# Performance work log

Hardware: AMD Instinct MI355X
Metric: run time of the kernel (lower is better)

Reference implementation:

```python
import jax, jax.numpy as jnp
import numpy as np

EPS = 1e-5

def _conv1d(x, w, b):
    # x: [N, Cin, L], w: [Cout, Cin, 3], SAME padding (pad=1)
    y = jax.lax.conv_general_dilated(
        x, w, window_strides=(1,), padding=((1, 1),),
        dimension_numbers=("NCH", "OIH", "NCH"))
    return y + b[None, :, None]

def _bn(x, gamma, beta, mean, var):
    # inference-mode BatchNorm1d over channel dim
    inv = gamma / jnp.sqrt(var + EPS)
    return x * inv[None, :, None] + (beta - mean * inv)[None, :, None]

def _make_params(key):
    ks = jax.random.split(key, 9)
    def w(k, o, i):
        return jax.random.normal(k, (o, i, 3), jnp.float32) * (1.0 / np.sqrt(i * 3))
    p = {}
    p["w1"], p["b1"] = w(ks[0], 128, 1), jnp.zeros((128,), jnp.float32)
    p["w2"], p["b2"] = w(ks[1], 256, 128), jnp.zeros((256,), jnp.float32)
    p["w3"], p["b3"] = w(ks[2], 256, 256), jnp.zeros((256,), jnp.float32)
    for i, c in zip((1, 2, 3), (128, 256, 256)):
        p[f"g{i}"] = jnp.ones((c,), jnp.float32)
        p[f"be{i}"] = jnp.zeros((c,), jnp.float32)
        p[f"m{i}"] = jax.random.normal(ks[2 + i], (c,), jnp.float32) * 0.1
        p[f"v{i}"] = 1.0 + 0.1 * jax.random.uniform(ks[5 + i], (c,), jnp.float32)
    return p

def setup_inputs() -> dict:
    key = jax.random.key(0)
    kx, kp = jax.random.split(key)
    inp = {"x": jax.random.normal(kx, (16, 64, 520), jnp.float32)}
    inp.update(_make_params(kp))
    return inp

def reference(x, w1, b1, w2, b2, w3, b3,
              g1, be1, m1, v1, g2, be2, m2, v2, g3, be3, m3, v3):
    B, T, D = x.shape
    h = x.reshape(B * T, 1, D)                     # fuse time into batch
    h = jax.nn.relu(_bn(_conv1d(h, w1, b1), g1, be1, m1, v1))
    h = jax.nn.relu(_bn(_conv1d(h, w2, b2), g2, be2, m2, v2))
    h = jax.nn.relu(_bn(_conv1d(h, w3, b3), g3, be3, m3, v3))
    out = h.mean(axis=-1)                          # AdaptiveAvgPool1d(1) + squeeze
    return out.reshape(B, T, -1)                   # [B, T, feature_dim]
```

## Files before the change

### kernel.cpp

```cpp
#include <hip/hip_runtime.h>
#include <hip/hip_bf16.h>

#define EPSV 1e-5f

typedef __attribute__((ext_vector_type(8))) short short8;
typedef __attribute__((ext_vector_type(4))) short short4v;
typedef __attribute__((ext_vector_type(4))) float f32x4;

static __device__ __forceinline__ short f2bf(float f) {
    unsigned int u = __builtin_bit_cast(unsigned int, f);
    unsigned int r = (u + 0x7FFFu + ((u >> 16) & 1u)) >> 16;
    return (short)(r & 0xFFFFu);
}
static __device__ __forceinline__ f32x4 zero4() { f32x4 z = {0.f, 0.f, 0.f, 0.f}; return z; }

static __device__ __forceinline__ void gload16(const void* g, void* l) {
    __builtin_amdgcn_global_load_lds((const unsigned int*)g, (unsigned int*)l, 16, 0, 0);
}

__global__ void sfe_prep(
    const float* __restrict__ w1, const float* __restrict__ b1,
    const float* __restrict__ w2, const float* __restrict__ b2,
    const float* __restrict__ w3, const float* __restrict__ b3,
    const float* __restrict__ g1, const float* __restrict__ be1,
    const float* __restrict__ m1, const float* __restrict__ v1,
    const float* __restrict__ g2, const float* __restrict__ be2,
    const float* __restrict__ m2, const float* __restrict__ v2,
    const float* __restrict__ g3, const float* __restrict__ be3,
    const float* __restrict__ m3, const float* __restrict__ v3,
    short* __restrict__ W2f, short* __restrict__ W3f,
    float* __restrict__ s1o, float* __restrict__ bb1o,
    float* __restrict__ bb2o, float* __restrict__ bb3o)
{
    int idx = blockIdx.x * 256 + threadIdx.x;
    int e = idx & 7, lane = (idx >> 3) & 63, ct = (idx >> 9) & 15;
    int lr = lane & 15, lg = lane >> 4;
    {
        int kc = idx >> 13;
        int c3 = ct * 16 + lr;
        int c2in = (kc & 7) * 32 + lg * 8 + e;
        int dk = kc >> 3;
        float s = g3[c3] / sqrtf(v3[c3] + EPSV);
        W3f[idx] = f2bf(w3[(c3 * 256 + c2in) * 3 + dk] * s);
    }
    if (idx < 98304) {
        int kc = idx >> 13;
        int c2 = ct * 16 + lr;
        int ci = (kc & 3) * 32 + lg * 8 + e;
        int dk = kc >> 2;
        float s = g2[c2] / sqrtf(v2[c2] + EPSV);
        W2f[idx] = f2bf(w2[(c2 * 128 + ci) * 3 + dk] * s);
    }
    if (idx < 128) {
        float s = g1[idx] / sqrtf(v1[idx] + EPSV);
        s1o[idx]  = s;
        bb1o[idx] = (b1[idx] - m1[idx]) * s + be1[idx];
    }
    if (idx < 256) {
        float s2 = g2[idx] / sqrtf(v2[idx] + EPSV);
        bb2o[idx] = (b2[idx] - m2[idx]) * s2 + be2[idx];
        float s3 = g3[idx] / sqrtf(v3[idx] + EPSV);
        bb3o[idx] = (b3[idx] - m3[idx]) * s3 + be3[idx];
    }
}

#define MFMA16(A, B, C) __builtin_amdgcn_mfma_f32_16x16x32_bf16(A, B, C, 0, 0, 0)

__global__ __launch_bounds__(512, 1) void sfe_l12(
    const float* __restrict__ x, const float* __restrict__ w1,
    const short* __restrict__ W2f,
    const float* __restrict__ s1a, const float* __restrict__ bb1a,
    const float* __restrict__ bb2a,
    char* __restrict__ h2g, int seq0)
{
    __shared__ __align__(16) char ring[32768];
    __shared__ __align__(16) char obuf[2][16384];
    __shared__ float xs[528];

    const int tid = threadIdx.x, lane = tid & 63, wid = tid >> 6;
    const int lr = lane & 15, lg = lane >> 4;
    const int seq = seq0 + blockIdx.x;
    char* h2b = h2g + (size_t)blockIdx.x * 270336;

    const int c4 = (tid & 31) * 4;
    float w1r[12];
    #pragma unroll
    for (int e2 = 0; e2 < 4; ++e2) {
        w1r[e2 * 3 + 0] = w1[(c4 + e2) * 3 + 0];
        w1r[e2 * 3 + 1] = w1[(c4 + e2) * 3 + 1];
        w1r[e2 * 3 + 2] = w1[(c4 + e2) * 3 + 2];
    }
    const f32x4 s1v = *reinterpret_cast<const f32x4*>(s1a + c4);
    const f32x4 b1v = *reinterpret_cast<const f32x4*>(bb1a + c4);

    short8 W2r[24];
    #pragma unroll
    for (int kc = 0; kc < 12; ++kc) {
        #pragma unroll
        for (int p = 0; p < 2; ++p)
            W2r[kc * 2 + p] = *reinterpret_cast<const short8*>(
                W2f + ((kc * 16 + wid * 2 + p) * 64 + lane) * 8);
    }
    const f32x4 bias0 = *reinterpret_cast<const f32x4*>(bb2a + (wid * 2 + 0) * 16 + lg * 4);
    const f32x4 bias1 = *reinterpret_cast<const f32x4*>(bb2a + (wid * 2 + 1) * 16 + lg * 4);

    for (int i = tid; i < 528; i += 512) {
        int l = i - 1;
        xs[i] = (l >= 0 && l < 520) ? x[(size_t)seq * 520 + l] : 0.f;
    }
    *reinterpret_cast<long long*>(ring + 28672 + tid * 8) = 0ll;
    __syncthreads();

    auto h1chunk = [&](int X) {
        int row = X * 16 + (tid >> 5);
        int rr = (row + 128) & 127;
        short4v hv;
        if (row < 520) {
            float x0 = xs[row], x1 = xs[row + 1], x2 = xs[row + 2];
            #pragma unroll
            for (int e2 = 0; e2 < 4; ++e2) {
                float a = w1r[e2 * 3] * x0 + w1r[e2 * 3 + 1] * x1 + w1r[e2 * 3 + 2] * x2;
                hv[e2] = f2bf(fmaxf(a * s1v[e2] + b1v[e2], 0.f));
            }
        } else {
            hv[0] = 0; hv[1] = 0; hv[2] = 0; hv[3] = 0;
        }
        int ch = c4 >> 3;
        *reinterpret_cast<short4v*>(
            ring + rr * 256 + ((ch ^ (row & 15)) << 4) + (c4 & 7) * 2) = hv;
    };

    h1chunk(0); h1chunk(1); h1chunk(2);
    __syncthreads();

    auto epi = [&](const f32x4& A, int p, const f32x4& bv, int jt, int b) {
        int c2b = (wid * 2 + p) * 16 + lg * 4;
        int ch = c2b >> 3;
        short4v hv;
        #pragma unroll
        for (int r = 0; r < 4; ++r) hv[r] = f2bf(fmaxf(A[r] + bv[r], 0.f));
        *reinterpret_cast<short4v*>(
            obuf[b] + (jt * 16 + lr) * 512 + ((ch ^ lr) << 4) + (c2b & 7) * 2) = hv;
    };

    for (int C = 0; C <= 32; C += 2) {
        const bool do2 = (C < 32);
        const int b = (C >> 1) & 1;
        f32x4 a00 = zero4(), a10 = zero4(), a01 = zero4(), a11 = zero4();
        const int row0base = C * 16 + lr - 1;

        if (do2) {
            #pragma unroll
            for (int kc = 0; kc < 12; ++kc) {
                int dk = kc >> 2, cc = kc & 3;
                int ch = cc * 4 + lg;
                int row0 = row0base + dk, row1 = row0 + 16;
                short8 B0 = *reinterpret_cast<const short8*>(
                    ring + ((row0 + 128) & 127) * 256 + ((ch ^ (row0 & 15)) << 4));
                short8 B1 = *reinterpret_cast<const short8*>(
                    ring + ((row1 + 128) & 127) * 256 + ((ch ^ (row1 & 15)) << 4));
                a00 = MFMA16(W2r[kc * 2 + 0], B0, a00);
                a10 = MFMA16(W2r[kc * 2 + 1], B0, a10);
                a01 = MFMA16(W2r[kc * 2 + 0], B1, a01);
                a11 = MFMA16(W2r[kc * 2 + 1], B1, a11);
            }
        } else {
            #pragma unroll
            for (int kc = 0; kc < 12; ++kc) {
                int dk = kc >> 2, cc = kc & 3;
                int ch = cc * 4 + lg;
                int row0 = row0base + dk;
                short8 B0 = *reinterpret_cast<const short8*>(
                    ring + ((row0 + 128) & 127) * 256 + ((ch ^ (row0 & 15)) << 4));
                a00 = MFMA16(W2r[kc * 2 + 0], B0, a00);
                a10 = MFMA16(W2r[kc * 2 + 1], B0, a10);
            }
        }

        if (C + 3 <= 32) h1chunk(C + 3);
        if (C + 4 <= 32) h1chunk(C + 4);

        epi(a00, 0, bias0, 0, b);
        epi(a10, 1, bias1, 0, b);
        if (do2) { epi(a01, 0, bias0, 1, b); epi(a11, 1, bias1, 1, b); }

        asm volatile("s_waitcnt lgkmcnt(0)" ::: "memory");
        __builtin_amdgcn_s_barrier();

        #pragma unroll
        for (int q = 0; q < 2; ++q) {
            int byteo = q * 8192 + tid * 16;
            int lrow = byteo >> 9;
            int grow = C * 16 + lrow;
            if (grow < 528 && (do2 || lrow < 16)) {
                short8 d = *reinterpret_cast<const short8*>(obuf[b] + byteo);
                if (grow >= 520) { short8 z = {0,0,0,0,0,0,0,0}; d = z; }
                *reinterpret_cast<short8*>(h2b + (size_t)grow * 512 + (byteo & 511)) = d;
            }
        }
    }
}

__global__ __launch_bounds__(256, 1) void sfe_l3(
    const char* __restrict__ h2g, const short* __restrict__ W3f,
    const float* __restrict__ bb3a, float* __restrict__ out, int seq0)
{
    __shared__ __align__(16) char ring[98304];

    const int tid = threadIdx.x, lane = tid & 63, wid = tid >> 6;
    const int lr = lane & 15, lg = lane >> 4;
    const int bi = blockIdx.x;
    const int seq = seq0 + (bi >> 1);
    const int ch2 = bi & 1;
    const char* h2b = h2g + (size_t)(bi >> 1) * 270336;

    short8 W3r[48];
    #pragma unroll
    for (int kc = 0; kc < 24; ++kc) {
        #pragma unroll
        for (int p = 0; p < 2; ++p)
            W3r[kc * 2 + p] = *reinterpret_cast<const short8*>(
                W3f + ((kc * 16 + ch2 * 8 + wid * 2 + p) * 64 + lane) * 8);
    }
    const f32x4 bias0 = *reinterpret_cast<const f32x4*>(bb3a + (ch2 * 8 + wid * 2 + 0) * 16 + lg * 4);
    const f32x4 bias1 = *reinterpret_cast<const f32x4*>(bb3a + (ch2 * 8 + wid * 2 + 1) * 16 + lg * 4);
    f32x4 pool0 = zero4(), pool1 = zero4();

    int Koff[24];
    #pragma unroll
    for (int kc = 0; kc < 24; ++kc) {
        int dk = kc >> 3, cc = kc & 7;
        Koff[kc] = (((cc * 4 + lg) ^ ((lr - 1 + dk) & 15)) << 4);
    }

    auto stage = [&](int X) {
        int Xc = X > 32 ? 32 : X;
        int slot = X % 12;
        #pragma unroll
        for (int q = 0; q < 2; ++q)
            gload16(h2b + Xc * 8192 + q * 4096 + tid * 16,
                    ring + slot * 8192 + q * 4096 + tid * 16);
    };

    #pragma unroll
    for (int q = 0; q < 2; ++q)
        *reinterpret_cast<f32x4*>(ring + 90112 + q * 4096 + tid * 16) = zero4();
    stage(0); stage(1); stage(2); stage(3); stage(4); stage(5); stage(6);
    asm volatile("s_waitcnt vmcnt(4) lgkmcnt(0)" ::: "memory");
    __builtin_amdgcn_s_barrier();

    #define RD(rbarr, KC, JT) \
        (*reinterpret_cast<const short8*>(ring + rbarr[(JT) * 3 + ((KC) >> 3)] + Koff[(KC)]))

    for (int S = 0; S <= 28; S += 4) {
        stage(S + 7); stage(S + 8); stage(S + 9); stage(S + 10);
        __builtin_amdgcn_sched_barrier(0);

        int rb[12];
        #pragma unroll
        for (int jt = 0; jt < 4; ++jt) {
            #pragma unroll
            for (int dk = 0; dk < 3; ++dk)
                rb[jt * 3 + dk] = (((S + jt) * 16 + lr - 1 + dk + 192) % 192) * 512;
        }

        f32x4 a0[4] = {zero4(), zero4(), zero4(), zero4()};
        f32x4 a1[4] = {zero4(), zero4(), zero4(), zero4()};
        short8 Ba[16], Bb[16];

        #define ISSUE(BUF, KCB) \
            _Pragma("unroll") for (int k = 0; k < 4; ++k) { \
                _Pragma("unroll") for (int jt = 0; jt < 4; ++jt) \
                    BUF[k * 4 + jt] = RD(rb, (KCB) + k, jt); \
            } \
            __builtin_amdgcn_sched_barrier(0);

        #define CONSUME(BUF, KCB) \
            _Pragma("unroll") for (int k = 0; k < 4; ++k) { \
                _Pragma("unroll") for (int jt = 0; jt < 4; ++jt) { \
                    a0[jt] = MFMA16(W3r[((KCB) + k) * 2 + 0], BUF[k * 4 + jt], a0[jt]); \
                    a1[jt] = MFMA16(W3r[((KCB) + k) * 2 + 1], BUF[k * 4 + jt], a1[jt]); \
                } \
            } \
            __builtin_amdgcn_sched_barrier(0);

        ISSUE(Ba, 0)
        ISSUE(Bb, 4)
        CONSUME(Ba, 0)
        ISSUE(Ba, 8)
        CONSUME(Bb, 4)
        ISSUE(Bb, 12)
        CONSUME(Ba, 8)
        ISSUE(Ba, 16)
        CONSUME(Bb, 12)
        ISSUE(Bb, 20)
        CONSUME(Ba, 16)
        CONSUME(Bb, 20)

        #undef ISSUE
        #undef CONSUME

        #pragma unroll
        for (int jt = 0; jt < 4; ++jt) {
            f32x4 t0, t1;
            #pragma unroll
            for (int r = 0; r < 4; ++r) {
                t0[r] = fmaxf(a0[jt][r] + bias0[r], 0.f);
                t1[r] = fmaxf(a1[jt][r] + bias1[r], 0.f);
            }
            pool0 += t0;
            pool1 += t1;
        }

        asm volatile("s_waitcnt vmcnt(4) lgkmcnt(0)" ::: "memory");
        __builtin_amdgcn_s_barrier();
    }

    {
        int rbT[3];
        #pragma unroll
        for (int dk = 0; dk < 3; ++dk)
            rbT[dk] = ((512 + lr - 1 + dk + 192) % 192) * 512;

        f32x4 a00 = zero4(), a10 = zero4();
        short8 Ta[12], Tb[12];
        #pragma unroll
        for (int k = 0; k < 12; ++k)
            Ta[k] = *reinterpret_cast<const short8*>(ring + rbT[k >> 3] + Koff[k]);
        __builtin_amdgcn_sched_barrier(0);
        #pragma unroll
        for (int k = 0; k < 12; ++k)
            Tb[k] = *reinterpret_cast<const short8*>(ring + rbT[(k + 12) >> 3] + Koff[k + 12]);
        __builtin_amdgcn_sched_barrier(0);
        #pragma unroll
        for (int k = 0; k < 12; ++k) {
            a00 = MFMA16(W3r[k * 2 + 0], Ta[k], a00);
            a10 = MFMA16(W3r[k * 2 + 1], Ta[k], a10);
        }
        #pragma unroll
        for (int k = 0; k < 12; ++k) {
            a00 = MFMA16(W3r[(k + 12) * 2 + 0], Tb[k], a00);
            a10 = MFMA16(W3r[(k + 12) * 2 + 1], Tb[k], a10);
        }

        bool v0 = (512 + lr) < 520;
        f32x4 t0, t1;
        #pragma unroll
        for (int r = 0; r < 4; ++r) {
            t0[r] = fmaxf(a00[r] + bias0[r], 0.f);
            t1[r] = fmaxf(a10[r] + bias1[r], 0.f);
        }
        pool0 += v0 ? t0 : zero4();
        pool1 += v0 ? t1 : zero4();
    }

    asm volatile("s_waitcnt vmcnt(0)" ::: "memory");

    #pragma unroll
    for (int d = 1; d < 16; d <<= 1) {
        #pragma unroll
        for (int r = 0; r < 4; ++r) {
            pool0[r] += __shfl_xor(pool0[r], d, 64);
            pool1[r] += __shfl_xor(pool1[r], d, 64);
        }
    }
    if (lr == 0) {
        f32x4 o0, o1;
        #pragma unroll
        for (int r = 0; r < 4; ++r) { o0[r] = pool0[r] * (1.f / 520.f); o1[r] = pool1[r] * (1.f / 520.f); }
        *reinterpret_cast<f32x4*>(out + (size_t)seq * 256 + (ch2 * 8 + wid * 2 + 0) * 16 + lg * 4) = o0;
        *reinterpret_cast<f32x4*>(out + (size_t)seq * 256 + (ch2 * 8 + wid * 2 + 1) * 16 + lg * 4) = o1;
    }
}

extern "C" void kernel_launch(void* const* d_in, const int* in_sizes, int n_in,
                              void* d_out, int out_size, void* d_ws, size_t ws_size,
                              hipStream_t stream) {
    (void)n_in; (void)out_size;
    const float* x   = (const float*)d_in[0];
    const float* w1  = (const float*)d_in[1];
    const float* b1  = (const float*)d_in[2];
    const float* w2  = (const float*)d_in[3];
    const float* b2  = (const float*)d_in[4];
    const float* w3  = (const float*)d_in[5];
    const float* b3  = (const float*)d_in[6];
    const float* g1  = (const float*)d_in[7];
    const float* be1 = (const float*)d_in[8];
    const float* m1  = (const float*)d_in[9];
    const float* v1  = (const float*)d_in[10];
    const float* g2  = (const float*)d_in[11];
    const float* be2 = (const float*)d_in[12];
    const float* m2  = (const float*)d_in[13];
    const float* v2  = (const float*)d_in[14];
    const float* g3  = (const float*)d_in[15];
    const float* be3 = (const float*)d_in[16];
    const float* m3  = (const float*)d_in[17];
    const float* v3  = (const float*)d_in[18];

    char* ws = (char*)d_ws;
    short* W2f  = (short*)(ws);
    short* W3f  = (short*)(ws + 196608);
    float* s1o  = (float*)(ws + 589824);
    float* bb1o = (float*)(ws + 590336);
    float* bb2o = (float*)(ws + 590848);
    float* bb3o = (float*)(ws + 591872);
    char*  h2g  = ws + (1 << 20);

    int nseq = in_sizes[0] / 520;
    size_t h2cap = ws_size > (size_t)(1 << 20) ? ws_size - (1 << 20) : 0;
    int maxseq = (int)(h2cap / 270336);
    if (maxseq < 1) maxseq = 1;
    if (maxseq > nseq) maxseq = nseq;

    sfe_prep<<<768, 256, 0, stream>>>(w1, b1, w2, b2, w3, b3,
                                      g1, be1, m1, v1, g2, be2, m2, v2,
                                      g3, be3, m3, v3,
                                      W2f, W3f, s1o, bb1o, bb2o, bb3o);
    for (int s0 = 0; s0 < nseq; s0 += maxseq) {
        int n = (nseq - s0) < maxseq ? (nseq - s0) : maxseq;
        sfe_l12<<<n, 512, 0, stream>>>(x, w1, W2f, s1o, bb1o, bb2o, h2g, s0);
        sfe_l3 <<<n * 2, 256, 0, stream>>>(h2g, W3f, bb3o, (float*)d_out, s0);
    }
}
```

Before: 427.2 us.

## Halve layer-2 block to 4 waves, each computing 4 channel tiles with batched LDS reads

Layer-1/2 kernel now uses 256 threads instead of 512. Each wave holds weights for four 16-channel output tiles (48 short8 registers) rather than two, so each B fragment read from LDS feeds four MFMAs. All 12 k-chunks of B are loaded up front, split into two halves separated by scheduling barriers, to overlap LDS latency with MFMA work. This cuts redundant LDS reads and barrier participants per block. In exchange it raises register pressure considerably and halves the waves available to hide latency, and the h1 production and output store loops are reworked to match the thread count.

```diff
diff --git a/kernel.cpp b/kernel.cpp
--- a/kernel.cpp
+++ b/kernel.cpp
@@ -66,7 +66,7 @@
 
 #define MFMA16(A, B, C) __builtin_amdgcn_mfma_f32_16x16x32_bf16(A, B, C, 0, 0, 0)
 
-__global__ __launch_bounds__(512, 1) void sfe_l12(
+__global__ __launch_bounds__(256, 1) void sfe_l12(
     const float* __restrict__ x, const float* __restrict__ w1,
     const short* __restrict__ W2f,
     const float* __restrict__ s1a, const float* __restrict__ bb1a,
@@ -83,6 +83,7 @@
     char* h2b = h2g + (size_t)blockIdx.x * 270336;
 
     const int c4 = (tid & 31) * 4;
+    const int chw = c4 >> 3;
     float w1r[12];
     #pragma unroll
     for (int e2 = 0; e2 < 4; ++e2) {
@@ -93,52 +94,56 @@
     const f32x4 s1v = *reinterpret_cast<const f32x4*>(s1a + c4);
     const f32x4 b1v = *reinterpret_cast<const f32x4*>(bb1a + c4);
 
-    short8 W2r[24];
+    short8 W2r[48];
     #pragma unroll
     for (int kc = 0; kc < 12; ++kc) {
         #pragma unroll
-        for (int p = 0; p < 2; ++p)
-            W2r[kc * 2 + p] = *reinterpret_cast<const short8*>(
-                W2f + ((kc * 16 + wid * 2 + p) * 64 + lane) * 8);
-    }
-    const f32x4 bias0 = *reinterpret_cast<const f32x4*>(bb2a + (wid * 2 + 0) * 16 + lg * 4);
-    const f32x4 bias1 = *reinterpret_cast<const f32x4*>(bb2a + (wid * 2 + 1) * 16 + lg * 4);
-
-    for (int i = tid; i < 528; i += 512) {
+        for (int p = 0; p < 4; ++p)
+            W2r[kc * 4 + p] = *reinterpret_cast<const short8*>(
+                W2f + ((kc * 16 + wid * 4 + p) * 64 + lane) * 8);
+    }
+    f32x4 bias[4];
+    #pragma unroll
+    for (int p = 0; p < 4; ++p)
+        bias[p] = *reinterpret_cast<const f32x4*>(bb2a + (wid * 4 + p) * 16 + lg * 4);
+
+    for (int i = tid; i < 528; i += 256) {
         int l = i - 1;
         xs[i] = (l >= 0 && l < 520) ? x[(size_t)seq * 520 + l] : 0.f;
     }
-    *reinterpret_cast<long long*>(ring + 28672 + tid * 8) = 0ll;
+    *reinterpret_cast<f32x4*>(ring + 28672 + tid * 16) = zero4();
     __syncthreads();
 
     auto h1chunk = [&](int X) {
-        int row = X * 16 + (tid >> 5);
-        int rr = (row + 128) & 127;
-        short4v hv;
-        if (row < 520) {
-            float x0 = xs[row], x1 = xs[row + 1], x2 = xs[row + 2];
-            #pragma unroll
-            for (int e2 = 0; e2 < 4; ++e2) {
-                float a = w1r[e2 * 3] * x0 + w1r[e2 * 3 + 1] * x1 + w1r[e2 * 3 + 2] * x2;
-                hv[e2] = f2bf(fmaxf(a * s1v[e2] + b1v[e2], 0.f));
-            }
-        } else {
-            hv[0] = 0; hv[1] = 0; hv[2] = 0; hv[3] = 0;
-        }
-        int ch = c4 >> 3;
-        *reinterpret_cast<short4v*>(
-            ring + rr * 256 + ((ch ^ (row & 15)) << 4) + (c4 & 7) * 2) = hv;
+        #pragma unroll
+        for (int rh = 0; rh < 2; ++rh) {
+            int row = X * 16 + rh * 8 + (tid >> 5);
+            int rr = row & 127;
+            short4v hv;
+            if (row < 520) {
+                float x0 = xs[row], x1 = xs[row + 1], x2 = xs[row + 2];
+                #pragma unroll
+                for (int e2 = 0; e2 < 4; ++e2) {
+                    float a = w1r[e2 * 3] * x0 + w1r[e2 * 3 + 1] * x1 + w1r[e2 * 3 + 2] * x2;
+                    hv[e2] = f2bf(fmaxf(a * s1v[e2] + b1v[e2], 0.f));
+                }
+            } else {
+                hv[0] = 0; hv[1] = 0; hv[2] = 0; hv[3] = 0;
+            }
+            *reinterpret_cast<short4v*>(
+                ring + rr * 256 + ((chw ^ (row & 15)) << 4) + (c4 & 7) * 2) = hv;
+        }
     };
 
     h1chunk(0); h1chunk(1); h1chunk(2);
     __syncthreads();
 
-    auto epi = [&](const f32x4& A, int p, const f32x4& bv, int jt, int b) {
-        int c2b = (wid * 2 + p) * 16 + lg * 4;
+    auto epi = [&](const f32x4& A, int p, int jt, int b) {
+        int c2b = (wid * 4 + p) * 16 + lg * 4;
         int ch = c2b >> 3;
         short4v hv;
         #pragma unroll
-        for (int r = 0; r < 4; ++r) hv[r] = f2bf(fmaxf(A[r] + bv[r], 0.f));
+        for (int r = 0; r < 4; ++r) hv[r] = f2bf(fmaxf(A[r] + bias[p][r], 0.f));
         *reinterpret_cast<short4v*>(
             obuf[b] + (jt * 16 + lr) * 512 + ((ch ^ lr) << 4) + (c2b & 7) * 2) = hv;
     };
@@ -146,50 +151,81 @@
     for (int C = 0; C <= 32; C += 2) {
         const bool do2 = (C < 32);
         const int b = (C >> 1) & 1;
-        f32x4 a00 = zero4(), a10 = zero4(), a01 = zero4(), a11 = zero4();
+        f32x4 a0[4] = {zero4(), zero4(), zero4(), zero4()};
+        f32x4 a1[4] = {zero4(), zero4(), zero4(), zero4()};
         const int row0base = C * 16 + lr - 1;
 
+        auto readB = [&](int kc, int jt) -> short8 {
+            int dk = kc >> 2, cc = kc & 3;
+            int ch = cc * 4 + lg;
+            int row = row0base + dk + jt * 16;
+            return *reinterpret_cast<const short8*>(
+                ring + ((row + 128) & 127) * 256 + ((ch ^ (row & 15)) << 4));
+        };
+
         if (do2) {
-            #pragma unroll
-            for (int kc = 0; kc < 12; ++kc) {
-                int dk = kc >> 2, cc = kc & 3;
-                int ch = cc * 4 + lg;
-                int row0 = row0base + dk, row1 = row0 + 16;
-                short8 B0 = *reinterpret_cast<const short8*>(
-                    ring + ((row0 + 128) & 127) * 256 + ((ch ^ (row0 & 15)) << 4));
-                short8 B1 = *reinterpret_cast<const short8*>(
-                    ring + ((row1 + 128) & 127) * 256 + ((ch ^ (row1 & 15)) << 4));
-                a00 = MFMA16(W2r[kc * 2 + 0], B0, a00);
-                a10 = MFMA16(W2r[kc * 2 + 1], B0, a10);
-                a01 = MFMA16(W2r[kc * 2 + 0], B1, a01);
-                a11 = MFMA16(W2r[kc * 2 + 1], B1, a11);
+            short8 B0a[6], B1a[6], B0b[6], B1b[6];
+            #pragma unroll
+            for (int k = 0; k < 6; ++k) { B0a[k] = readB(k, 0); B1a[k] = readB(k, 1); }
+            __builtin_amdgcn_sched_barrier(0);
+            #pragma unroll
+            for (int k = 0; k < 6; ++k) { B0b[k] = readB(k + 6, 0); B1b[k] = readB(k + 6, 1); }
+            __builtin_amdgcn_sched_barrier(0);
+            #pragma unroll
+            for (int k = 0; k < 6; ++k) {
+                #pragma unroll
+                for (int p = 0; p < 4; ++p) {
+                    a0[p] = MFMA16(W2r[k * 4 + p], B0a[k], a0[p]);
+                    a1[p] = MFMA16(W2r[k * 4 + p], B1a[k], a1[p]);
+                }
+            }
+            __builtin_amdgcn_sched_barrier(0);
+            #pragma unroll
+            for (int k = 0; k < 6; ++k) {
+                #pragma unroll
+                for (int p = 0; p < 4; ++p) {
+                    a0[p] = MFMA16(W2r[(k + 6) * 4 + p], B0b[k], a0[p]);
+                    a1[p] = MFMA16(W2r[(k + 6) * 4 + p], B1b[k], a1[p]);
+                }
             }
         } else {
-            #pragma unroll
-            for (int kc = 0; kc < 12; ++kc) {
-                int dk = kc >> 2, cc = kc & 3;
-                int ch = cc * 4 + lg;
-                int row0 = row0base + dk;
-                short8 B0 = *reinterpret_cast<const short8*>(
-                    ring + ((row0 + 128) & 127) * 256 + ((ch ^ (row0 & 15)) << 4));
-                a00 = MFMA16(W2r[kc * 2 + 0], B0, a00);
-                a10 = MFMA16(W2r[kc * 2 + 1], B0, a10);
+            short8 B0a[6], B0b[6];
+            #pragma unroll
+            for (int k = 0; k < 6; ++k) B0a[k] = readB(k, 0);
+            __builtin_amdgcn_sched_barrier(0);
+            #pragma unroll
+            for (int k = 0; k < 6; ++k) B0b[k] = readB(k + 6, 0);
+            __builtin_amdgcn_sched_barrier(0);
+            #pragma unroll
+            for (int k = 0; k < 6; ++k) {
+                #pragma unroll
+                for (int p = 0; p < 4; ++p)
+                    a0[p] = MFMA16(W2r[k * 4 + p], B0a[k], a0[p]);
+            }
+            #pragma unroll
+            for (int k = 0; k < 6; ++k) {
+                #pragma unroll
+                for (int p = 0; p < 4; ++p)
+                    a0[p] = MFMA16(W2r[(k + 6) * 4 + p], B0b[k], a0[p]);
             }
         }
 
         if (C + 3 <= 32) h1chunk(C + 3);
         if (C + 4 <= 32) h1chunk(C + 4);
 
-        epi(a00, 0, bias0, 0, b);
-        epi(a10, 1, bias1, 0, b);
-        if (do2) { epi(a01, 0, bias0, 1, b); epi(a11, 1, bias1, 1, b); }
+        #pragma unroll
+        for (int p = 0; p < 4; ++p) epi(a0[p], p, 0, b);
+        if (do2) {
+            #pragma unroll
+            for (int p = 0; p < 4; ++p) epi(a1[p], p, 1, b);
+        }
 
         asm volatile("s_waitcnt lgkmcnt(0)" ::: "memory");
         __builtin_amdgcn_s_barrier();
 
         #pragma unroll
-        for (int q = 0; q < 2; ++q) {
-            int byteo = q * 8192 + tid * 16;
+        for (int q = 0; q < 4; ++q) {
+            int byteo = q * 4096 + tid * 16;
             int lrow = byteo >> 9;
             int grow = C * 16 + lrow;
             if (grow < 528 && (do2 || lrow < 16)) {
@@ -418,7 +454,7 @@
                                       W2f, W3f, s1o, bb1o, bb2o, bb3o);
     for (int s0 = 0; s0 < nseq; s0 += maxseq) {
         int n = (nseq - s0) < maxseq ? (nseq - s0) : maxseq;
-        sfe_l12<<<n, 512, 0, stream>>>(x, w1, W2f, s1o, bb1o, bb2o, h2g, s0);
+        sfe_l12<<<n, 256, 0, stream>>>(x, w1, W2f, s1o, bb1o, bb2o, h2g, s0);
         sfe_l3 <<<n * 2, 256, 0, stream>>>(h2g, W3f, bb3o, (float*)d_out, s0);
     }
 }
```

New measurement: 480.6 us. +12.5%, slower.
